# Kernel optimization log

Hardware: AMD Instinct MI355X
Metric: run time of the kernel (lower is better)

## Reference

```python
import jax, jax.numpy as jnp
import numpy as np

B, L, H = 4, 1024, 1024
NH, HD = 16, 64
ND = NH * HD
ITERS = 4
U = 5  # MSA1 ring window size (hard-coded in source)


def _conv1x1(w, b, x):  # w [O,C], b [O], x [B,C,L] -> [B,O,L]  (Conv2d 1x1 == per-position linear)
    return jnp.einsum('oc,bcl->bol', w, x) + b[None, :, None]


def _layernorm(x, s, b, eps=1e-5):  # x [B,H,L]; LayerNorm over channel dim H
    mu = x.mean(1, keepdims=True)
    var = ((x - mu) ** 2).mean(1, keepdims=True)
    return (x - mu) / jnp.sqrt(var + eps) * s[None, :, None] + b[None, :, None]


def _msa1(x, ax, wq, bq, wk, bk, wv, bv, wo, bo):
    # x [B,H,L] normalized nodes; ax [B,H,2,L] (ring embedding + relay)
    b, h, l = x.shape
    q = _conv1x1(wq, bq, x).reshape(b, NH, HD, l)
    k = _conv1x1(wk, bk, x).reshape(b, NH, HD, l)
    v = _conv1x1(wv, bv, x).reshape(b, NH, HD, l)
    pad = U // 2
    kp = jnp.pad(k, ((0, 0), (0, 0), (0, 0), (pad, pad)))
    vp = jnp.pad(v, ((0, 0), (0, 0), (0, 0), (pad, pad)))
    # F.unfold with (U,1) kernel along L == stack of U shifted views
    kw = jnp.stack([kp[..., u:u + l] for u in range(U)], axis=3)  # [B,NH,HD,U,L]
    vw = jnp.stack([vp[..., u:u + l] for u in range(U)], axis=3)
    al = ax.shape[2]
    ak = (jnp.einsum('oc,bcal->boal', wk, ax) + bk[None, :, None, None]).reshape(b, NH, HD, al, l)
    av = (jnp.einsum('oc,bcal->boal', wv, ax) + bv[None, :, None, None]).reshape(b, NH, HD, al, l)
    kw = jnp.concatenate([kw, ak], axis=3)  # [B,NH,HD,U+2,L]
    vw = jnp.concatenate([vw, av], axis=3)
    scores = (q[:, :, :, None, :] * kw).sum(2) / np.sqrt(HD)  # [B,NH,U+2,L]
    alphas = jax.nn.softmax(scores, axis=2)
    att = (alphas[:, :, None, :, :] * vw).sum(3).reshape(b, ND, l)
    return _conv1x1(wo, bo, att)  # [B,H,L]


def _msa2(relay, y, smask, wq, bq, wk, bk, wo, bo):
    # relay [B,H]; y [B,H,L+1]; smask [B,L+1] True at padding
    b = relay.shape[0]
    q = (jnp.einsum('oc,bc->bo', wq, relay) + bq).reshape(b, NH, HD)
    k = _conv1x1(wk, bk, y).reshape(b, NH, HD, -1)
    pre = jnp.einsum('bnd,bndl->bnl', q, k) / np.sqrt(HD)
    pre = jnp.where(smask[:, None, :], -1e10, pre)
    alphas = jax.nn.softmax(pre, axis=-1)
    # NOTE: source has v = k (WV output unused) -- reproduced faithfully
    att = jnp.einsum('bnl,bndl->bnd', alphas, k).reshape(b, ND)
    return jnp.einsum('oc,bc->bo', wo, att) + bo  # [B,H]


def _star_forward(data, mask, ln_s, ln_b, rwq, rwq_b, rwk, rwk_b, rwv, rwv_b, rwo, rwo_b,
                  swq, swq_b, swk, swk_b, swo, swo_b):
    b, l, h = data.shape
    pad_mask = (mask == 0)  # True at padding positions
    smask = jnp.concatenate([jnp.zeros((b, 1), bool), pad_mask], axis=1)  # [B,L+1]
    embs = jnp.transpose(data, (0, 2, 1))  # [B,H,L]
    nodes = embs
    relay = embs.mean(2)  # [B,H]
    for i in range(ITERS):
        xn = _layernorm(nodes, ln_s[i], ln_b[i])
        ax = jnp.stack([embs, jnp.broadcast_to(relay[:, :, None], embs.shape)], axis=2)  # [B,H,2,L]
        ring = _msa1(xn, ax, rwq[i], rwq_b[i], rwk[i], rwk_b[i], rwv[i], rwv_b[i], rwo[i], rwo_b[i])
        nodes = nodes + jax.nn.leaky_relu(ring)
        y = jnp.concatenate([relay[:, :, None], nodes], axis=2)  # [B,H,L+1]
        relay = jax.nn.leaky_relu(_msa2(relay, y, smask, swq[i], swq_b[i], swk[i], swk_b[i], swo[i], swo_b[i]))
        nodes = jnp.where(pad_mask[:, None, :], 0.0, nodes)
    return jnp.transpose(nodes, (0, 2, 1)), relay  # [B,L,H], [B,H]


def setup_inputs() -> dict:
    key = jax.random.key(0)
    ks = jax.random.split(key, 16)
    def p(k, shape):
        return jax.random.normal(k, shape, jnp.float32) * 0.02
    return dict(
        data=jax.random.normal(ks[0], (B, L, H), jnp.float32),
        mask=jax.random.randint(ks[1], (B, L), 0, 2).astype(jnp.int32),
        ln_s=jnp.ones((ITERS, H), jnp.float32),
        ln_b=jnp.zeros((ITERS, H), jnp.float32),
        rwq=p(ks[2], (ITERS, ND, H)), rwq_b=p(ks[3], (ITERS, ND)),
        rwk=p(ks[4], (ITERS, ND, H)), rwk_b=p(ks[5], (ITERS, ND)),
        rwv=p(ks[6], (ITERS, ND, H)), rwv_b=p(ks[7], (ITERS, ND)),
        rwo=p(ks[8], (ITERS, H, ND)), rwo_b=p(ks[9], (ITERS, H)),
        swq=p(ks[10], (ITERS, ND, H)), swq_b=p(ks[11], (ITERS, ND)),
        swk=p(ks[12], (ITERS, ND, H)), swk_b=p(ks[13], (ITERS, ND)),
        swo=p(ks[14], (ITERS, H, ND)), swo_b=p(ks[15], (ITERS, H)),
    )


def reference(data, mask, ln_s, ln_b, rwq, rwq_b, rwk, rwk_b, rwv, rwv_b, rwo, rwo_b,
              swq, swq_b, swk, swk_b, swo, swo_b):
    return _star_forward(data, mask, ln_s, ln_b, rwq, rwq_b, rwk, rwk_b, rwv, rwv_b,
                         rwo, rwo_b, swq, swq_b, swk, swk_b, swo, swo_b)
```

## Files before the change

### kernel.cpp

```cpp
#include <hip/hip_runtime.h>
#include <math.h>

namespace {

constexpr int B_ = 4, L_ = 1024, H_ = 1024, NH_ = 16, HD_ = 64, ND_ = 1024, ITERS_ = 4;

typedef unsigned short u16;
typedef __attribute__((ext_vector_type(8))) short short8;
typedef __attribute__((ext_vector_type(4))) float f32x4;

__device__ inline u16 f2bf(float f) {
  unsigned u = __builtin_bit_cast(unsigned, f);
  u += 0x7FFFu + ((u >> 16) & 1u);
  return (u16)(u >> 16);
}
__device__ inline float bf2f(u16 v) {
  unsigned u = ((unsigned)v) << 16;
  return __builtin_bit_cast(float, u);
}

__device__ inline void gl_lds16(const u16* g, u16* l) {
  __builtin_amdgcn_global_load_lds((const __attribute__((address_space(1))) void*)g,
                                   (__attribute__((address_space(3))) void*)l, 16, 0, 0);
}

__global__ void k_prep(const float* __restrict__ data, const float* __restrict__ rwq,
                       const float* __restrict__ rwk, const float* __restrict__ rwv,
                       const float* __restrict__ rwo, const float* __restrict__ swk,
                       u16* __restrict__ embs_bf, u16* __restrict__ wq_bf,
                       u16* __restrict__ wk_bf, u16* __restrict__ wv_bf,
                       u16* __restrict__ wo_bf, u16* __restrict__ swk_bf,
                       float* __restrict__ nodes) {
  int i = blockIdx.x * 256 + threadIdx.x;
  int which = blockIdx.y;
  if (which == 6) {
    reinterpret_cast<float4*>(nodes)[i] = reinterpret_cast<const float4*>(data)[i];
    return;
  }
  const float* src;
  u16* dst;
  switch (which) {
    case 0: src = data; dst = embs_bf; break;
    case 1: src = rwq; dst = wq_bf; break;
    case 2: src = rwk; dst = wk_bf; break;
    case 3: src = rwv; dst = wv_bf; break;
    case 4: src = rwo; dst = wo_bf; break;
    default: src = swk; dst = swk_bf; break;
  }
  float4 v = reinterpret_cast<const float4*>(src)[i];
  ushort4 o;
  o.x = f2bf(v.x); o.y = f2bf(v.y); o.z = f2bf(v.z); o.w = f2bf(v.w);
  reinterpret_cast<ushort4*>(dst)[i] = o;
}

__global__ void k_relay_part(const float* __restrict__ data, float* __restrict__ part) {
  int b = blockIdx.z, chunk = blockIdx.y;
  int c = blockIdx.x * 256 + threadIdx.x;
  const float* p = data + ((size_t)b * L_ + chunk * 128) * H_ + c;
  float acc = 0.f;
  for (int l = 0; l < 128; ++l) acc += p[(size_t)l * H_];
  part[((size_t)b * 8 + chunk) * H_ + c] = acc;
}
__global__ void k_relay_reduce(const float* __restrict__ part, float* __restrict__ relay) {
  int i = blockIdx.x * 256 + threadIdx.x;
  int b = i >> 10, c = i & 1023;
  float acc = 0.f;
  for (int j = 0; j < 8; ++j) acc += part[((size_t)b * 8 + j) * H_ + c];
  relay[i] = acc * (1.f / (float)L_);
}

__global__ __launch_bounds__(256) void k_layernorm_bf(float* __restrict__ nodes,
                                                      const float* __restrict__ s,
                                                      const float* __restrict__ bb,
                                                      const int* __restrict__ mask,
                                                      u16* __restrict__ y, int do_zero) {
  int row = blockIdx.x * 4 + (threadIdx.x >> 6);
  int lane = threadIdx.x & 63;
  int b = row >> 10, l = row & 1023;
  bool pad = do_zero && (mask[b * L_ + l] == 0);
  float4* xr = reinterpret_cast<float4*>(nodes + (size_t)row * H_);
  float4 v[4];
  float sum = 0.f, sq = 0.f;
#pragma unroll
  for (int j = 0; j < 4; ++j) {
    v[j] = pad ? float4{0.f, 0.f, 0.f, 0.f} : xr[lane + 64 * j];
    sum += v[j].x + v[j].y + v[j].z + v[j].w;
    sq += v[j].x * v[j].x + v[j].y * v[j].y + v[j].z * v[j].z + v[j].w * v[j].w;
  }
  if (pad) {
#pragma unroll
    for (int j = 0; j < 4; ++j) xr[lane + 64 * j] = float4{0.f, 0.f, 0.f, 0.f};
  }
#pragma unroll
  for (int off = 32; off; off >>= 1) {
    sum += __shfl_xor(sum, off);
    sq += __shfl_xor(sq, off);
  }
  float mu = sum * (1.f / (float)H_);
  float rstd = rsqrtf(sq * (1.f / (float)H_) - mu * mu + 1e-5f);
  ushort4* yr = reinterpret_cast<ushort4*>(y + (size_t)row * H_);
#pragma unroll
  for (int j = 0; j < 4; ++j) {
    int c4 = lane + 64 * j;
    float4 sc = reinterpret_cast<const float4*>(s)[c4];
    float4 bc = reinterpret_cast<const float4*>(bb)[c4];
    ushort4 o;
    o.x = f2bf((v[j].x - mu) * rstd * sc.x + bc.x);
    o.y = f2bf((v[j].y - mu) * rstd * sc.y + bc.y);
    o.z = f2bf((v[j].z - mu) * rstd * sc.z + bc.z);
    o.w = f2bf((v[j].w - mu) * rstd * sc.w + bc.w);
    yr[c4] = o;
  }
}


#define GEMM_PROLOGUE(XPTR, WPTR)                                              \
  __shared__ __align__(16) u16 sX[2][128 * 32];                                \
  __shared__ __align__(16) u16 sW[2][128 * 32];                                \
  const int t = threadIdx.x;                                                   \
  const int w = t >> 6, lane = t & 63;                                         \
  const int wm = w >> 1, wn = w & 1;                                           \
  const int r4 = lane >> 2, slot = lane & 3;                                   \
  const int rowS0 = w * 16 + r4, rowS1 = 64 + rowS0;                           \
  const int colS0 = ((slot ^ ((rowS0 >> 1) & 3)) << 3);                        \
  const int colS1 = ((slot ^ ((rowS1 >> 1) & 3)) << 3);                        \
  const u16* gX0 = (XPTR) + (size_t)(bm + rowS0) * 1024 + colS0;               \
  const u16* gX1 = (XPTR) + (size_t)(bm + rowS1) * 1024 + colS1;               \
  const u16* gW0 = (WPTR) + (size_t)(bn + rowS0) * 1024 + colS0;               \
  const u16* gW1 = (WPTR) + (size_t)(bn + rowS1) * 1024 + colS1;               \
  const int kidx = (((lane >> 4) ^ ((lane >> 1) & 3)) << 3);                   \
  f32x4 acc[4][4];                                                             \
  _Pragma("unroll") for (int i_ = 0; i_ < 4; ++i_)                             \
      _Pragma("unroll") for (int j_ = 0; j_ < 4; ++j_)                         \
          acc[i_][j_] = f32x4{0.f, 0.f, 0.f, 0.f};

#define GEMM_STAGE(BUF)                                                        \
  gl_lds16(gX0, sX[BUF] + w * 512);                                            \
  gl_lds16(gX1, sX[BUF] + (4 + w) * 512);                                      \
  gl_lds16(gW0, sW[BUF] + w * 512);                                            \
  gl_lds16(gW1, sW[BUF] + (4 + w) * 512);                                      \
  gX0 += 32; gX1 += 32; gW0 += 32; gW1 += 32;

#define GEMM_KLOOP_DB(AROWBASE, BROWBASE, ASRC, BSRC)                          \
  int cur = 0;                                                                 \
  GEMM_STAGE(0)                                                                \
  for (int ck = 0; ck < 1024; ck += 32) {                                      \
    if (ck < 992) {                                                            \
      GEMM_STAGE(cur ^ 1)                                                      \
      asm volatile("s_waitcnt vmcnt(4)" ::: "memory");                         \
    } else {                                                                   \
      asm volatile("s_waitcnt vmcnt(0)" ::: "memory");                         \
    }                                                                          \
    __builtin_amdgcn_s_barrier();                                              \
    __builtin_amdgcn_sched_barrier(0);                                         \
    short8 af_[4], bf_[4];                                                     \
    _Pragma("unroll") for (int mf = 0; mf < 4; ++mf)                           \
        af_[mf] = *reinterpret_cast<const short8*>(                            \
            &ASRC[cur][((AROWBASE) + mf * 16) * 32 + kidx]);                   \
    _Pragma("unroll") for (int nf = 0; nf < 4; ++nf)                           \
        bf_[nf] = *reinterpret_cast<const short8*>(                            \
            &BSRC[cur][((BROWBASE) + nf * 16) * 32 + kidx]);                   \
    _Pragma("unroll") for (int mf = 0; mf < 4; ++mf)                           \
        _Pragma("unroll") for (int nf = 0; nf < 4; ++nf)                       \
            acc[mf][nf] = __builtin_amdgcn_mfma_f32_16x16x32_bf16(             \
                af_[mf], bf_[nf], acc[mf][nf], 0, 0, 0);                       \
    __builtin_amdgcn_sched_barrier(0);                                         \
    __builtin_amdgcn_s_barrier();                                              \
    cur ^= 1;                                                                  \
  }

__global__ __launch_bounds__(256) void k_gemm5(const u16* __restrict__ wq,
                                               const u16* __restrict__ wk,
                                               const u16* __restrict__ wv,
                                               const float* __restrict__ bq,
                                               const float* __restrict__ bk,
                                               const float* __restrict__ bv,
                                               const u16* __restrict__ xn,
                                               const u16* __restrict__ embs,
                                               u16* __restrict__ Y) {
  const int bm = blockIdx.x * 128;
  const int which = blockIdx.y >> 3;
  const int bn = (blockIdx.y & 7) * 128;
  const u16* W = (which == 0) ? wq : ((which == 1 || which == 3) ? wk : wv);
  const float* bias = (which == 0) ? bq : ((which == 1 || which == 3) ? bk : bv);
  const u16* X = (which < 3) ? xn : embs;
  u16* Yw = Y + (size_t)which * ((size_t)B_ * L_ * ND_);

  GEMM_PROLOGUE(X, W)
  const int rW = wm * 64 + (lane & 15);
  const int rX = wn * 64 + (lane & 15);
  GEMM_KLOOP_DB(rW, rX, sW, sX)

#pragma unroll
  for (int mo = 0; mo < 4; ++mo) {
    int o0 = bn + wm * 64 + mo * 16 + ((lane >> 4) << 2);
    float4 bs = *reinterpret_cast<const float4*>(bias + o0);
#pragma unroll
    for (int nl = 0; nl < 4; ++nl) {
      int bl = bm + wn * 64 + nl * 16 + (lane & 15);
      f32x4 vv = acc[mo][nl];
      ushort4 ov;
      ov.x = f2bf(vv[0] + bs.x);
      ov.y = f2bf(vv[1] + bs.y);
      ov.z = f2bf(vv[2] + bs.z);
      ov.w = f2bf(vv[3] + bs.w);
      *reinterpret_cast<ushort4*>(&Yw[(size_t)bl * 1024 + o0]) = ov;
    }
  }
}

__global__ __launch_bounds__(256) void k_gemm_wo(const u16* __restrict__ W,
                                                 const float* __restrict__ bias,
                                                 const u16* __restrict__ X,
                                                 float* __restrict__ nodes,
                                                 u16* __restrict__ nodes_bf) {
  const int bm = blockIdx.x * 128;
  const int bn = blockIdx.y * 128;
  GEMM_PROLOGUE(X, W)
  const int rW = wm * 64 + (lane & 15);
  const int rX = wn * 64 + (lane & 15);
  GEMM_KLOOP_DB(rW, rX, sW, sX)

#pragma unroll
  for (int mo = 0; mo < 4; ++mo) {
    int o0 = bn + wm * 64 + mo * 16 + ((lane >> 4) << 2);
    float4 bs = *reinterpret_cast<const float4*>(bias + o0);
#pragma unroll
    for (int nl = 0; nl < 4; ++nl) {
      int bl = bm + wn * 64 + nl * 16 + (lane & 15);
      size_t ni = (size_t)bl * 1024 + o0;
      float4 curv = *reinterpret_cast<const float4*>(&nodes[ni]);
      f32x4 vv = acc[mo][nl];
      float r0 = vv[0] + bs.x; r0 = curv.x + (r0 > 0.f ? r0 : 0.01f * r0);
      float r1 = vv[1] + bs.y; r1 = curv.y + (r1 > 0.f ? r1 : 0.01f * r1);
      float r2 = vv[2] + bs.z; r2 = curv.z + (r2 > 0.f ? r2 : 0.01f * r2);
      float r3 = vv[3] + bs.w; r3 = curv.w + (r3 > 0.f ? r3 : 0.01f * r3);
      *reinterpret_cast<float4*>(&nodes[ni]) = float4{r0, r1, r2, r3};
      ushort4 ov;
      ov.x = f2bf(r0); ov.y = f2bf(r1); ov.z = f2bf(r2); ov.w = f2bf(r3);
      *reinterpret_cast<ushort4*>(&nodes_bf[ni]) = ov;
    }
  }
}

__global__ __launch_bounds__(256) void k_gemm_kkb(const u16* __restrict__ W,
                                                  const float* __restrict__ bias,
                                                  const u16* __restrict__ X,
                                                  float* __restrict__ Y) {
  const int bm = blockIdx.x * 128;
  const int bn = blockIdx.y * 128;
  GEMM_PROLOGUE(X, W)
  const int rX = wm * 64 + (lane & 15);
  const int rW = wn * 64 + (lane & 15);
  GEMM_KLOOP_DB(rX, rW, sX, sW)

#pragma unroll
  for (int nf = 0; nf < 4; ++nf) {
    int o = bn + wn * 64 + nf * 16 + (lane & 15);
    float bs = bias[o];
#pragma unroll
    for (int mf = 0; mf < 4; ++mf) {
      int gl = bm + wm * 64 + mf * 16 + ((lane >> 4) << 2);
      int b = gl >> 10, l = gl & 1023;
      size_t yi = ((size_t)(b * 1024 + o)) * (size_t)(L_ + 1) + 1 + l;
      f32x4 v = acc[mf][nf];
#pragma unroll
      for (int r = 0; r < 4; ++r) Y[yi + r] = v[r] + bs;
    }
  }
}

__global__ __launch_bounds__(256) void k_matvec2(const float* __restrict__ W0,
                                                 const float* __restrict__ b0,
                                                 float* __restrict__ y0, long sB0, long sO0,
                                                 const float* __restrict__ W1,
                                                 const float* __restrict__ b1,
                                                 float* __restrict__ y1, long sB1, long sO1,
                                                 const float* __restrict__ x) {
  int b = blockIdx.y;
  int z = blockIdx.z;
  const float* W = z ? W1 : W0;
  const float* bias = z ? b1 : b0;
  float* y = z ? y1 : y0;
  long sB = z ? sB1 : sB0, sO = z ? sO1 : sO0;
  int o = blockIdx.x * 4 + (threadIdx.x >> 6);
  int lane = threadIdx.x & 63;
  const float* wr = W + (size_t)o * 1024;
  const float* xb = x + (size_t)b * 1024;
  float acc = 0.f;
  for (int c = lane; c < 1024; c += 64) acc += wr[c] * xb[c];
#pragma unroll
  for (int off = 32; off; off >>= 1) acc += __shfl_xor(acc, off);
  if (lane == 0) y[(size_t)b * sB + (size_t)o * sO] = acc + bias[o];
}

__global__ __launch_bounds__(256) void k_matvec(const float* __restrict__ W,
                                                const float* __restrict__ bias,
                                                const float* __restrict__ x,
                                                float* __restrict__ y) {
  int b = blockIdx.y;
  int o = blockIdx.x * 4 + (threadIdx.x >> 6);
  int lane = threadIdx.x & 63;
  const float* wr = W + (size_t)o * 1024;
  const float* xb = x + (size_t)b * 1024;
  float acc = 0.f;
  for (int c = lane; c < 1024; c += 64) acc += wr[c] * xb[c];
#pragma unroll
  for (int off = 32; off; off >>= 1) acc += __shfl_xor(acc, off);
  if (lane == 0) {
    acc += bias[o];
    y[(size_t)b * 1024 + o] = acc > 0.f ? acc : 0.01f * acc;
  }
}

__global__ __launch_bounds__(256) void k_msa1(const u16* __restrict__ q,
                                              const u16* __restrict__ k,
                                              const u16* __restrict__ v,
                                              const u16* __restrict__ ke,
                                              const u16* __restrict__ ve,
                                              const float* __restrict__ rk,
                                              const float* __restrict__ rv,
                                              u16* __restrict__ attbf) {
  int t = threadIdx.x;
  int head = t & 15, dh = (t >> 4) & 1, lsub = t >> 5;
  int l = blockIdx.x * 8 + lsub;
  int b = blockIdx.z;
  size_t row = ((size_t)(b * 1024 + l)) * 1024 + head * 64 + dh * 32;
  size_t rbase = (size_t)b * 1024 + head * 64 + dh * 32;

  float qf[32];
  {
    const short8* qp = reinterpret_cast<const short8*>(q + row);
#pragma unroll
    for (int j = 0; j < 4; ++j) {
      short8 qv = qp[j];
#pragma unroll
      for (int e = 0; e < 8; ++e) qf[j * 8 + e] = bf2f((u16)qv[e]);
    }
  }
  float s[7];
#pragma unroll
  for (int u = 0; u < 5; ++u) {
    int lk = l + u - 2;
    float su = 0.f;
    if (lk >= 0 && lk < L_) {
      const short8* kp =
          reinterpret_cast<const short8*>(k + ((size_t)(b * 1024 + lk)) * 1024 + head * 64 + dh * 32);
#pragma unroll
      for (int j = 0; j < 4; ++j) {
        short8 kv = kp[j];
#pragma unroll
        for (int e = 0; e < 8; ++e) su = fmaf(qf[j * 8 + e], bf2f((u16)kv[e]), su);
      }
    }
    s[u] = su;
  }
  {
    float su = 0.f;
    const short8* kp = reinterpret_cast<const short8*>(ke + row);
#pragma unroll
    for (int j = 0; j < 4; ++j) {
      short8 kv = kp[j];
#pragma unroll
      for (int e = 0; e < 8; ++e) su = fmaf(qf[j * 8 + e], bf2f((u16)kv[e]), su);
    }
    s[5] = su;
  }
  {
    float su = 0.f;
    const float4* rp = reinterpret_cast<const float4*>(rk + rbase);
#pragma unroll
    for (int j = 0; j < 8; ++j) {
      float4 r4 = rp[j];
      su = fmaf(qf[j * 4 + 0], r4.x, su);
      su = fmaf(qf[j * 4 + 1], r4.y, su);
      su = fmaf(qf[j * 4 + 2], r4.z, su);
      su = fmaf(qf[j * 4 + 3], r4.w, su);
    }
    s[6] = su;
  }
#pragma unroll
  for (int u = 0; u < 7; ++u) s[u] += __shfl_xor(s[u], 16);
  float m = -1e30f;
#pragma unroll
  for (int u = 0; u < 7; ++u) {
    s[u] *= 0.125f;
    m = fmaxf(m, s[u]);
  }
  float e[7], tot = 0.f;
#pragma unroll
  for (int u = 0; u < 7; ++u) {
    e[u] = expf(s[u] - m);
    tot += e[u];
  }
  float inv = 1.f / tot;
#pragma unroll
  for (int u = 0; u < 7; ++u) e[u] *= inv;

  float av[32];
  {
    const float4* rp = reinterpret_cast<const float4*>(rv + rbase);
#pragma unroll
    for (int j = 0; j < 8; ++j) {
      float4 r4 = rp[j];
      av[j * 4 + 0] = e[6] * r4.x;
      av[j * 4 + 1] = e[6] * r4.y;
      av[j * 4 + 2] = e[6] * r4.z;
      av[j * 4 + 3] = e[6] * r4.w;
    }
  }
  {
    const short8* vp = reinterpret_cast<const short8*>(ve + row);
#pragma unroll
    for (int j = 0; j < 4; ++j) {
      short8 vv = vp[j];
#pragma unroll
      for (int ee = 0; ee < 8; ++ee) av[j * 8 + ee] = fmaf(e[5], bf2f((u16)vv[ee]), av[j * 8 + ee]);
    }
  }
#pragma unroll
  for (int u = 0; u < 5; ++u) {
    int lk = l + u - 2;
    if (lk >= 0 && lk < L_) {
      const short8* vp =
          reinterpret_cast<const short8*>(v + ((size_t)(b * 1024 + lk)) * 1024 + head * 64 + dh * 32);
#pragma unroll
      for (int j = 0; j < 4; ++j) {
        short8 vv = vp[j];
#pragma unroll
        for (int ee = 0; ee < 8; ++ee) av[j * 8 + ee] = fmaf(e[u], bf2f((u16)vv[ee]), av[j * 8 + ee]);
      }
    }
  }
  u16 ob[32];
#pragma unroll
  for (int j = 0; j < 32; ++j) ob[j] = f2bf(av[j]);
  uint4* d4 = reinterpret_cast<uint4*>(attbf + row);
  const uint4* s4 = reinterpret_cast<const uint4*>(ob);
#pragma unroll
  for (int j = 0; j < 4; ++j) d4[j] = s4[j];
}

__global__ __launch_bounds__(256) void k_msa2p(const float* __restrict__ rq,
                                               const float* __restrict__ kk,
                                               const int* __restrict__ mask,
                                               float* __restrict__ pw,
                                               float* __restrict__ pE) {
  int n = blockIdx.x, c = blockIdx.y, b = blockIdx.z;
  int tid = threadIdx.x;
  __shared__ float sq_[HD_];
  __shared__ float se[260];
  size_t rb = (size_t)(b * NH_ + n) * HD_;
  if (tid < HD_) sq_[tid] = rq[rb + tid];
  __syncthreads();
  const float* kb = kk + rb * (size_t)(L_ + 1);
  int p0 = c * 256;
  {
    int p = p0 + tid;
    float e;
    if (p > 0 && mask[b * L_ + p - 1] == 0) {
      e = 0.f;
    } else {
      float acc = 0.f;
      for (int d = 0; d < HD_; ++d) acc = fmaf(sq_[d], kb[(size_t)d * (L_ + 1) + p], acc);
      e = expf(acc * 0.125f);
    }
    se[tid] = e;
  }
  int nP = 256;
  if (c == 3) {
    nP = 257;
    if (tid == 0) {
      float e;
      if (mask[b * L_ + 1023] == 0) {
        e = 0.f;
      } else {
        float acc = 0.f;
        for (int d = 0; d < HD_; ++d) acc = fmaf(sq_[d], kb[(size_t)d * (L_ + 1) + 1024], acc);
        e = expf(acc * 0.125f);
      }
      se[256] = e;
    }
  }
  __syncthreads();
  int lane = tid & 63, w = tid >> 6;
  if (w == 0) {
    float E = 0.f;
    for (int i = lane; i < nP; i += 64) E += se[i];
#pragma unroll
    for (int off = 32; off; off >>= 1) E += __shfl_xor(E, off);
    if (lane == 0) pE[((size_t)(b * NH_ + n)) * 4 + c] = E;
  }
  for (int dd = 0; dd < 16; ++dd) {
    int d = w * 16 + dd;
    const float* kd = kb + (size_t)d * (L_ + 1) + p0;
    float a = 0.f;
    for (int i = lane; i < nP; i += 64) a = fmaf(se[i], kd[i], a);
#pragma unroll
    for (int off = 32; off; off >>= 1) a += __shfl_xor(a, off);
    if (lane == 0) pw[(((size_t)(b * NH_ + n)) * 4 + c) * HD_ + d] = a;
  }
}

__global__ void k_msa2r(const float* __restrict__ pw, const float* __restrict__ pE,
                        float* __restrict__ satt) {
  int i = blockIdx.x * 256 + threadIdx.x;
  int bn = i >> 6, d = i & 63;
  float E = pE[bn * 4 + 0] + pE[bn * 4 + 1] + pE[bn * 4 + 2] + pE[bn * 4 + 3];
  float ws = pw[((size_t)bn * 4 + 0) * HD_ + d] + pw[((size_t)bn * 4 + 1) * HD_ + d] +
             pw[((size_t)bn * 4 + 2) * HD_ + d] + pw[((size_t)bn * 4 + 3) * HD_ + d];
  satt[i] = ws / E;
}

__global__ void k_final(const float* __restrict__ nodes, const int* __restrict__ mask,
                        float* __restrict__ out) {
  int i = blockIdx.x * 256 + threadIdx.x;
  int row = i >> 8;
  int b = row >> 10, l = row & 1023;
  float4 v = (mask[b * L_ + l] == 0) ? float4{0.f, 0.f, 0.f, 0.f}
                                     : reinterpret_cast<const float4*>(nodes)[i];
  reinterpret_cast<float4*>(out)[i] = v;
}

__global__ void k_copy_relay(const float* __restrict__ relay, float* __restrict__ out) {
  int i = blockIdx.x * 256 + threadIdx.x;
  out[i] = relay[i];
}

}

extern "C" void kernel_launch(void* const* d_in, const int* in_sizes, int n_in,
                              void* d_out, int out_size, void* d_ws, size_t ws_size,
                              hipStream_t stream) {
  (void)in_sizes; (void)n_in; (void)out_size; (void)ws_size;
  const float* data = (const float*)d_in[0];
  const int* mask = (const int*)d_in[1];
  const float* ln_s = (const float*)d_in[2];
  const float* ln_b = (const float*)d_in[3];
  const float* rwq = (const float*)d_in[4];
  const float* rwq_b = (const float*)d_in[5];
  const float* rwk = (const float*)d_in[6];
  const float* rwk_b = (const float*)d_in[7];
  const float* rwv = (const float*)d_in[8];
  const float* rwv_b = (const float*)d_in[9];
  const float* rwo = (const float*)d_in[10];
  const float* rwo_b = (const float*)d_in[11];
  const float* swq = (const float*)d_in[12];
  const float* swq_b = (const float*)d_in[13];
  const float* swk = (const float*)d_in[14];
  const float* swk_b = (const float*)d_in[15];
  const float* swo = (const float*)d_in[16];
  const float* swo_b = (const float*)d_in[17];
  float* out = (float*)d_out;

  const size_t SZ = (size_t)B_ * ND_ * L_;
  float* f = (float*)d_ws;
  float* nodes = f; f += SZ;
  float* kkb = f; f += (size_t)B_ * ND_ * (L_ + 1);
  float* part = f; f += (size_t)B_ * 8 * H_;
  float* relay = f; f += B_ * H_;
  float* rk = f; f += B_ * ND_;
  float* rv = f; f += B_ * ND_;
  float* rq = f; f += B_ * ND_;
  float* satt = f; f += B_ * ND_;
  float* pw = f; f += (size_t)B_ * NH_ * 4 * HD_;
  float* pE = f; f += B_ * NH_ * 4;
  u16* u = (u16*)f;
  u16* xn_bf = u; u += SZ;
  u16* embs_bf = u; u += SZ;
  u16* att_bf = u; u += SZ;
  u16* nodes_bf = u; u += SZ;
  u16* qkv5_bf = u; u += 5 * SZ;
  u16* wq_bf = u; u += SZ;
  u16* wk_bf = u; u += SZ;
  u16* wv_bf = u; u += SZ;
  u16* wo_bf = u; u += SZ;
  u16* swk_bf = u; u += SZ;

  k_prep<<<dim3(4096, 7), 256, 0, stream>>>(data, rwq, rwk, rwv, rwo, swk,
                                            embs_bf, wq_bf, wk_bf, wv_bf, wo_bf, swk_bf, nodes);
  k_relay_part<<<dim3(H_ / 256, 8, B_), 256, 0, stream>>>(data, part);
  k_relay_reduce<<<dim3((B_ * H_) / 256), 256, 0, stream>>>(part, relay);

  for (int i = 0; i < ITERS_; ++i) {
    const u16* wq_i = wq_bf + (size_t)i * ND_ * H_;
    const u16* wk_i = wk_bf + (size_t)i * ND_ * H_;
    const u16* wv_i = wv_bf + (size_t)i * ND_ * H_;
    const u16* wo_i = wo_bf + (size_t)i * H_ * ND_;
    const u16* sk_i = swk_bf + (size_t)i * ND_ * H_;

    k_layernorm_bf<<<dim3(B_ * L_ / 4), 256, 0, stream>>>(nodes, ln_s + i * H_, ln_b + i * H_,
                                                          mask, xn_bf, i > 0 ? 1 : 0);
    k_gemm5<<<dim3(32, 40), 256, 0, stream>>>(wq_i, wk_i, wv_i,
                                              rwq_b + i * ND_, rwk_b + i * ND_, rwv_b + i * ND_,
                                              xn_bf, embs_bf, qkv5_bf);
    k_matvec2<<<dim3(256, B_, 2), 256, 0, stream>>>(
        rwk + (size_t)i * ND_ * H_, rwk_b + i * ND_, rk, ND_, 1,
        rwv + (size_t)i * ND_ * H_, rwv_b + i * ND_, rv, ND_, 1, relay);
    k_msa1<<<dim3(L_ / 8, 1, B_), 256, 0, stream>>>(qkv5_bf, qkv5_bf + SZ, qkv5_bf + 2 * SZ,
                                                    qkv5_bf + 3 * SZ, qkv5_bf + 4 * SZ, rk, rv, att_bf);
    k_gemm_wo<<<dim3(32, 8), 256, 0, stream>>>(wo_i, rwo_b + i * H_, att_bf, nodes, nodes_bf);
    k_matvec2<<<dim3(256, B_, 2), 256, 0, stream>>>(
        swq + (size_t)i * ND_ * H_, swq_b + i * ND_, rq, ND_, 1,
        swk + (size_t)i * ND_ * H_, swk_b + i * ND_, kkb, (long)ND_ * (L_ + 1), L_ + 1, relay);
    k_gemm_kkb<<<dim3(32, 8), 256, 0, stream>>>(sk_i, swk_b + i * ND_, nodes_bf, kkb);
    k_msa2p<<<dim3(NH_, 4, B_), 256, 0, stream>>>(rq, kkb, mask, pw, pE);
    k_msa2r<<<dim3((B_ * NH_ * HD_) / 256), 256, 0, stream>>>(pw, pE, satt);
    k_matvec<<<dim3(256, B_), 256, 0, stream>>>(swo + (size_t)i * H_ * ND_, swo_b + i * H_, satt, relay);
  }
  k_final<<<4096, 256, 0, stream>>>(nodes, mask, out);
  k_copy_relay<<<dim3((B_ * H_) / 256), 256, 0, stream>>>(relay, out + (size_t)B_ * L_ * H_);
}
```

Before: 764.2 us.

## Rework GEMM k-loop to 64-wide single stage, swizzle blocks, remap msa1 threads

```diff
diff --git a/kernel.cpp b/kernel.cpp
--- a/kernel.cpp
+++ b/kernel.cpp
@@ -128,59 +128,63 @@
   const u16* gX1 = (XPTR) + (size_t)(bm + rowS1) * 1024 + colS1;               \
   const u16* gW0 = (WPTR) + (size_t)(bn + rowS0) * 1024 + colS0;               \
   const u16* gW1 = (WPTR) + (size_t)(bn + rowS1) * 1024 + colS1;               \
+  u16* lX0a = sX[0] + w * 512;                                                 \
+  u16* lX0b = sX[1] + w * 512;                                                 \
+  u16* lX1a = sX[0] + (4 + w) * 512;                                           \
+  u16* lX1b = sX[1] + (4 + w) * 512;                                           \
+  u16* lW0a = sW[0] + w * 512;                                                 \
+  u16* lW0b = sW[1] + w * 512;                                                 \
+  u16* lW1a = sW[0] + (4 + w) * 512;                                           \
+  u16* lW1b = sW[1] + (4 + w) * 512;                                           \
   const int kidx = (((lane >> 4) ^ ((lane >> 1) & 3)) << 3);                   \
   f32x4 acc[4][4];                                                             \
   _Pragma("unroll") for (int i_ = 0; i_ < 4; ++i_)                             \
       _Pragma("unroll") for (int j_ = 0; j_ < 4; ++j_)                         \
           acc[i_][j_] = f32x4{0.f, 0.f, 0.f, 0.f};
 
-#define GEMM_STAGE(BUF)                                                        \
-  gl_lds16(gX0, sX[BUF] + w * 512);                                            \
-  gl_lds16(gX1, sX[BUF] + (4 + w) * 512);                                      \
-  gl_lds16(gW0, sW[BUF] + w * 512);                                            \
-  gl_lds16(gW1, sW[BUF] + (4 + w) * 512);                                      \
-  gX0 += 32; gX1 += 32; gW0 += 32; gW1 += 32;
-
-#define GEMM_KLOOP_DB(AROWBASE, BROWBASE, ASRC, BSRC)                          \
-  int cur = 0;                                                                 \
-  GEMM_STAGE(0)                                                                \
-  for (int ck = 0; ck < 1024; ck += 32) {                                      \
-    if (ck < 992) {                                                            \
-      GEMM_STAGE(cur ^ 1)                                                      \
-      asm volatile("s_waitcnt vmcnt(4)" ::: "memory");                         \
-    } else {                                                                   \
-      asm volatile("s_waitcnt vmcnt(0)" ::: "memory");                         \
+#define GEMM_KLOOP64(AROWBASE, BROWBASE, ASRC, BSRC)                           \
+  for (int ck = 0; ck < 1024; ck += 64) {                                      \
+    gl_lds16(gX0, lX0a);                                                       \
+    gl_lds16(gX0 + 32, lX0b);                                                  \
+    gl_lds16(gX1, lX1a);                                                       \
+    gl_lds16(gX1 + 32, lX1b);                                                  \
+    gl_lds16(gW0, lW0a);                                                       \
+    gl_lds16(gW0 + 32, lW0b);                                                  \
+    gl_lds16(gW1, lW1a);                                                       \
+    gl_lds16(gW1 + 32, lW1b);                                                  \
+    gX0 += 64; gX1 += 64; gW0 += 64; gW1 += 64;                                \
+    __syncthreads();                                                           \
+    _Pragma("unroll") for (int h = 0; h < 2; ++h) {                            \
+      short8 af_[4], bf_[4];                                                   \
+      _Pragma("unroll") for (int mf = 0; mf < 4; ++mf)                         \
+          af_[mf] = *reinterpret_cast<const short8*>(                          \
+              &ASRC[h][((AROWBASE) + mf * 16) * 32 + kidx]);                   \
+      _Pragma("unroll") for (int nf = 0; nf < 4; ++nf)                         \
+          bf_[nf] = *reinterpret_cast<const short8*>(                          \
+              &BSRC[h][((BROWBASE) + nf * 16) * 32 + kidx]);                   \
+      _Pragma("unroll") for (int mf = 0; mf < 4; ++mf)                         \
+          _Pragma("unroll") for (int nf = 0; nf < 4; ++nf)                     \
+              acc[mf][nf] = __builtin_amdgcn_mfma_f32_16x16x32_bf16(           \
+                  af_[mf], bf_[nf], acc[mf][nf], 0, 0, 0);                     \
     }                                                                          \
-    __builtin_amdgcn_s_barrier();                                              \
-    __builtin_amdgcn_sched_barrier(0);                                         \
-    short8 af_[4], bf_[4];                                                     \
-    _Pragma("unroll") for (int mf = 0; mf < 4; ++mf)                           \
-        af_[mf] = *reinterpret_cast<const short8*>(                            \
-            &ASRC[cur][((AROWBASE) + mf * 16) * 32 + kidx]);                   \
-    _Pragma("unroll") for (int nf = 0; nf < 4; ++nf)                           \
-        bf_[nf] = *reinterpret_cast<const short8*>(                            \
-            &BSRC[cur][((BROWBASE) + nf * 16) * 32 + kidx]);                   \
-    _Pragma("unroll") for (int mf = 0; mf < 4; ++mf)                           \
-        _Pragma("unroll") for (int nf = 0; nf < 4; ++nf)                       \
-            acc[mf][nf] = __builtin_amdgcn_mfma_f32_16x16x32_bf16(             \
-                af_[mf], bf_[nf], acc[mf][nf], 0, 0, 0);                       \
-    __builtin_amdgcn_sched_barrier(0);                                         \
-    __builtin_amdgcn_s_barrier();                                              \
-    cur ^= 1;                                                                  \
-  }
-
-__global__ __launch_bounds__(256) void k_gemm5(const u16* __restrict__ wq,
-                                               const u16* __restrict__ wk,
-                                               const u16* __restrict__ wv,
-                                               const float* __restrict__ bq,
-                                               const float* __restrict__ bk,
-                                               const float* __restrict__ bv,
-                                               const u16* __restrict__ xn,
-                                               const u16* __restrict__ embs,
-                                               u16* __restrict__ Y) {
-  const int bm = blockIdx.x * 128;
-  const int which = blockIdx.y >> 3;
-  const int bn = (blockIdx.y & 7) * 128;
+    __syncthreads();                                                          \
+  }
+
+__global__ __launch_bounds__(256, 3) void k_gemm5(const u16* __restrict__ wq,
+                                                  const u16* __restrict__ wk,
+                                                  const u16* __restrict__ wv,
+                                                  const float* __restrict__ bq,
+                                                  const float* __restrict__ bk,
+                                                  const float* __restrict__ bv,
+                                                  const u16* __restrict__ xn,
+                                                  const u16* __restrict__ embs,
+                                                  u16* __restrict__ Y) {
+  const int orig = blockIdx.y * 32 + blockIdx.x;
+  const int swz = (orig & 7) * 160 + (orig >> 3);
+  const int sbx = swz & 31, sby = swz >> 5;
+  const int bm = sbx * 128;
+  const int which = sby >> 3;
+  const int bn = (sby & 7) * 128;
   const u16* W = (which == 0) ? wq : ((which == 1 || which == 3) ? wk : wv);
   const float* bias = (which == 0) ? bq : ((which == 1 || which == 3) ? bk : bv);
   const u16* X = (which < 3) ? xn : embs;
@@ -189,7 +193,7 @@
   GEMM_PROLOGUE(X, W)
   const int rW = wm * 64 + (lane & 15);
   const int rX = wn * 64 + (lane & 15);
-  GEMM_KLOOP_DB(rW, rX, sW, sX)
+  GEMM_KLOOP64(rW, rX, sW, sX)
 
 #pragma unroll
   for (int mo = 0; mo < 4; ++mo) {
@@ -209,17 +213,19 @@
   }
 }
 
-__global__ __launch_bounds__(256) void k_gemm_wo(const u16* __restrict__ W,
-                                                 const float* __restrict__ bias,
-                                                 const u16* __restrict__ X,
-                                                 float* __restrict__ nodes,
-                                                 u16* __restrict__ nodes_bf) {
-  const int bm = blockIdx.x * 128;
-  const int bn = blockIdx.y * 128;
+__global__ __launch_bounds__(256, 3) void k_gemm_wo(const u16* __restrict__ W,
+                                                    const float* __restrict__ bias,
+                                                    const u16* __restrict__ X,
+                                                    float* __restrict__ nodes,
+                                                    u16* __restrict__ nodes_bf) {
+  const int orig = blockIdx.y * 32 + blockIdx.x;
+  const int swz = (orig & 7) * 32 + (orig >> 3);
+  const int bm = (swz & 31) * 128;
+  const int bn = (swz >> 5) * 128;
   GEMM_PROLOGUE(X, W)
   const int rW = wm * 64 + (lane & 15);
   const int rX = wn * 64 + (lane & 15);
-  GEMM_KLOOP_DB(rW, rX, sW, sX)
+  GEMM_KLOOP64(rW, rX, sW, sX)
 
 #pragma unroll
   for (int mo = 0; mo < 4; ++mo) {
@@ -243,16 +249,18 @@
   }
 }
 
-__global__ __launch_bounds__(256) void k_gemm_kkb(const u16* __restrict__ W,
-                                                  const float* __restrict__ bias,
-                                                  const u16* __restrict__ X,
-                                                  float* __restrict__ Y) {
-  const int bm = blockIdx.x * 128;
-  const int bn = blockIdx.y * 128;
+__global__ __launch_bounds__(256, 3) void k_gemm_kkb(const u16* __restrict__ W,
+                                                     const float* __restrict__ bias,
+                                                     const u16* __restrict__ X,
+                                                     float* __restrict__ Y) {
+  const int orig = blockIdx.y * 32 + blockIdx.x;
+  const int swz = (orig & 7) * 32 + (orig >> 3);
+  const int bm = (swz & 31) * 128;
+  const int bn = (swz >> 5) * 128;
   GEMM_PROLOGUE(X, W)
   const int rX = wm * 64 + (lane & 15);
   const int rW = wn * 64 + (lane & 15);
-  GEMM_KLOOP_DB(rX, rW, sX, sW)
+  GEMM_KLOOP64(rX, rW, sX, sW)
 
 #pragma unroll
   for (int nf = 0; nf < 4; ++nf) {
@@ -297,7 +305,7 @@
 __global__ __launch_bounds__(256) void k_matvec(const float* __restrict__ W,
                                                 const float* __restrict__ bias,
                                                 const float* __restrict__ x,
-                                                float* __restrict__ y) {
+                                                float* __restrict__ y, int leaky) {
   int b = blockIdx.y;
   int o = blockIdx.x * 4 + (threadIdx.x >> 6);
   int lane = threadIdx.x & 63;
@@ -309,7 +317,8 @@
   for (int off = 32; off; off >>= 1) acc += __shfl_xor(acc, off);
   if (lane == 0) {
     acc += bias[o];
-    y[(size_t)b * 1024 + o] = acc > 0.f ? acc : 0.01f * acc;
+    if (leaky) acc = acc > 0.f ? acc : 0.01f * acc;
+    y[(size_t)b * 1024 + o] = acc;
   }
 }
 
@@ -322,17 +331,18 @@
                                               const float* __restrict__ rv,
                                               u16* __restrict__ attbf) {
   int t = threadIdx.x;
-  int head = t & 15, dh = (t >> 4) & 1, lsub = t >> 5;
-  int l = blockIdx.x * 8 + lsub;
+  int wv = t >> 6, lane = t & 63;
+  int head = lane >> 2, dq = lane & 3;
+  int l = blockIdx.x * 4 + wv;
   int b = blockIdx.z;
-  size_t row = ((size_t)(b * 1024 + l)) * 1024 + head * 64 + dh * 32;
-  size_t rbase = (size_t)b * 1024 + head * 64 + dh * 32;
-
-  float qf[32];
+  size_t row = ((size_t)(b * 1024 + l)) * 1024 + head * 64 + dq * 16;
+  size_t rbase = (size_t)b * 1024 + head * 64 + dq * 16;
+
+  float qf[16];
   {
     const short8* qp = reinterpret_cast<const short8*>(q + row);
 #pragma unroll
-    for (int j = 0; j < 4; ++j) {
+    for (int j = 0; j < 2; ++j) {
       short8 qv = qp[j];
 #pragma unroll
       for (int e = 0; e < 8; ++e) qf[j * 8 + e] = bf2f((u16)qv[e]);
@@ -344,10 +354,10 @@
     int lk = l + u - 2;
     float su = 0.f;
     if (lk >= 0 && lk < L_) {
-      const short8* kp =
-          reinterpret_cast<const short8*>(k + ((size_t)(b * 1024 + lk)) * 1024 + head * 64 + dh * 32);
-#pragma unroll
-      for (int j = 0; j < 4; ++j) {
+      const short8* kp = reinterpret_cast<const short8*>(
+          k + ((size_t)(b * 1024 + lk)) * 1024 + head * 64 + dq * 16);
+#pragma unroll
+      for (int j = 0; j < 2; ++j) {
         short8 kv = kp[j];
 #pragma unroll
         for (int e = 0; e < 8; ++e) su = fmaf(qf[j * 8 + e], bf2f((u16)kv[e]), su);
@@ -359,7 +369,7 @@
     float su = 0.f;
     const short8* kp = reinterpret_cast<const short8*>(ke + row);
 #pragma unroll
-    for (int j = 0; j < 4; ++j) {
+    for (int j = 0; j < 2; ++j) {
       short8 kv = kp[j];
 #pragma unroll
       for (int e = 0; e < 8; ++e) su = fmaf(qf[j * 8 + e], bf2f((u16)kv[e]), su);
@@ -370,7 +380,7 @@
     float su = 0.f;
     const float4* rp = reinterpret_cast<const float4*>(rk + rbase);
 #pragma unroll
-    for (int j = 0; j < 8; ++j) {
+    for (int j = 0; j < 4; ++j) {
       float4 r4 = rp[j];
       su = fmaf(qf[j * 4 + 0], r4.x, su);
       su = fmaf(qf[j * 4 + 1], r4.y, su);
@@ -380,7 +390,10 @@
     s[6] = su;
   }
 #pragma unroll
-  for (int u = 0; u < 7; ++u) s[u] += __shfl_xor(s[u], 16);
+  for (int u = 0; u < 7; ++u) {
+    s[u] += __shfl_xor(s[u], 1);
+    s[u] += __shfl_xor(s[u], 2);
+  }
   float m = -1e30f;
 #pragma unroll
   for (int u = 0; u < 7; ++u) {
@@ -397,11 +410,11 @@
 #pragma unroll
   for (int u = 0; u < 7; ++u) e[u] *= inv;
 
-  float av[32];
+  float av[16];
   {
     const float4* rp = reinterpret_cast<const float4*>(rv + rbase);
 #pragma unroll
-    for (int j = 0; j < 8; ++j) {
+    for (int j = 0; j < 4; ++j) {
       float4 r4 = rp[j];
       av[j * 4 + 0] = e[6] * r4.x;
       av[j * 4 + 1] = e[6] * r4.y;
@@ -412,33 +425,33 @@
   {
     const short8* vp = reinterpret_cast<const short8*>(ve + row);
 #pragma unroll
-    for (int j = 0; j < 4; ++j) {
-      short8 vv = vp[j];
-#pragma unroll
-      for (int ee = 0; ee < 8; ++ee) av[j * 8 + ee] = fmaf(e[5], bf2f((u16)vv[ee]), av[j * 8 + ee]);
+    for (int j = 0; j < 2; ++j) {
+      short8 vvv = vp[j];
+#pragma unroll
+      for (int ee = 0; ee < 8; ++ee) av[j * 8 + ee] = fmaf(e[5], bf2f((u16)vvv[ee]), av[j * 8 + ee]);
     }
   }
 #pragma unroll
   for (int u = 0; u < 5; ++u) {
     int lk = l + u - 2;
     if (lk >= 0 && lk < L_) {
-      const short8* vp =
-          reinterpret_cast<const short8*>(v + ((size_t)(b * 1024 + lk)) * 1024 + head * 64 + dh * 32);
-#pragma unroll
-      for (int j = 0; j < 4; ++j) {
-        short8 vv = vp[j];
-#pragma unroll
-        for (int ee = 0; ee < 8; ++ee) av[j * 8 + ee] = fmaf(e[u], bf2f((u16)vv[ee]), av[j * 8 + ee]);
+      const short8* vp = reinterpret_cast<const short8*>(
+          v + ((size_t)(b * 1024 + lk)) * 1024 + head * 64 + dq * 16);
+#pragma unroll
+      for (int j = 0; j < 2; ++j) {
+        short8 vvv = vp[j];
+#pragma unroll
+        for (int ee = 0; ee < 8; ++ee) av[j * 8 + ee] = fmaf(e[u], bf2f((u16)vvv[ee]), av[j * 8 + ee]);
       }
     }
   }
-  u16 ob[32];
-#pragma unroll
-  for (int j = 0; j < 32; ++j) ob[j] = f2bf(av[j]);
+  u16 ob[16];
+#pragma unroll
+  for (int j = 0; j < 16; ++j) ob[j] = f2bf(av[j]);
   uint4* d4 = reinterpret_cast<uint4*>(attbf + row);
   const uint4* s4 = reinterpret_cast<const uint4*>(ob);
-#pragma unroll
-  for (int j = 0; j < 4; ++j) d4[j] = s4[j];
+  d4[0] = s4[0];
+  d4[1] = s4[1];
 }
 
 __global__ __launch_bounds__(256) void k_msa2p(const float* __restrict__ rq,
@@ -597,7 +610,7 @@
     k_matvec2<<<dim3(256, B_, 2), 256, 0, stream>>>(
         rwk + (size_t)i * ND_ * H_, rwk_b + i * ND_, rk, ND_, 1,
         rwv + (size_t)i * ND_ * H_, rwv_b + i * ND_, rv, ND_, 1, relay);
-    k_msa1<<<dim3(L_ / 8, 1, B_), 256, 0, stream>>>(qkv5_bf, qkv5_bf + SZ, qkv5_bf + 2 * SZ,
+    k_msa1<<<dim3(L_ / 4, 1, B_), 256, 0, stream>>>(qkv5_bf, qkv5_bf + SZ, qkv5_bf + 2 * SZ,
                                                     qkv5_bf + 3 * SZ, qkv5_bf + 4 * SZ, rk, rv, att_bf);
     k_gemm_wo<<<dim3(32, 8), 256, 0, stream>>>(wo_i, rwo_b + i * H_, att_bf, nodes, nodes_bf);
     k_matvec2<<<dim3(256, B_, 2), 256, 0, stream>>>(
@@ -606,7 +619,8 @@
     k_gemm_kkb<<<dim3(32, 8), 256, 0, stream>>>(sk_i, swk_b + i * ND_, nodes_bf, kkb);
     k_msa2p<<<dim3(NH_, 4, B_), 256, 0, stream>>>(rq, kkb, mask, pw, pE);
     k_msa2r<<<dim3((B_ * NH_ * HD_) / 256), 256, 0, stream>>>(pw, pE, satt);
-    k_matvec<<<dim3(256, B_), 256, 0, stream>>>(swo + (size_t)i * H_ * ND_, swo_b + i * H_, satt, relay);
+    k_matvec<<<dim3(256, B_), 256, 0, stream>>>(swo + (size_t)i * H_ * ND_, swo_b + i * H_,
+                                                satt, relay, 1);
   }
   k_final<<<4096, 256, 0, stream>>>(nodes, mask, out);
   k_copy_relay<<<dim3((B_ * H_) / 256), 256, 0, stream>>>(relay, out + (size_t)B_ * L_ * H_);
```

Result: faster. 711.7 us (-6.9%).
